# Optimization experiments

Hardware: AMD Instinct MI355X
Metric: run time of the kernel (lower is better)

The kernel has to match this reference:

```python
import jax, jax.numpy as jnp
import numpy as np

B, T, D, H, L, S = 128, 100, 256, 512, 40000, 10  # batch, steps, input_size, hidden_size, loc_count, num_slots


def setup_inputs() -> dict:
    key = jax.random.key(0)
    ks = jax.random.split(key, 24)
    stdv = 1.0 / np.sqrt(H)
    u = lambda k, shape: jax.random.uniform(k, shape, jnp.float32, -stdv, stdv)
    inp = {
        "batch_l": jax.random.randint(ks[0], (B, T), 0, L),
        "t_ld": jax.random.uniform(ks[1], (B, T), jnp.float32),
        "t_hd": jax.random.uniform(ks[2], (B, T), jnp.float32),
        "t_l": jax.random.randint(ks[3], (B, T), 0, S),
        "t_h": jax.random.randint(ks[4], (B, T), 0, S),
        "d_ld": jax.random.uniform(ks[5], (B, T), jnp.float32),
        "d_hd": jax.random.uniform(ks[6], (B, T), jnp.float32),
        "d_l": jax.random.randint(ks[7], (B, T), 0, S),
        "d_h": jax.random.randint(ks[8], (B, T), 0, S),
        # learned parameters
        "embed_l": jax.random.normal(ks[9], (L, D), jnp.float32) * 0.02,
        "embed_s": jax.random.normal(ks[10], (S, D), jnp.float32) * 0.02,
        "embed_q": jax.random.normal(ks[11], (S, D), jnp.float32) * 0.02,
        "w_ih": u(ks[12], (4 * H, D)),
        "w_hh": u(ks[13], (4 * H, H)),
        "w_s": u(ks[14], (3 * H, D)),
        "w_q": u(ks[15], (3 * H, D)),
        "b_ih": u(ks[16], (4 * H,)),
        "b_hh": u(ks[17], (4 * H,)),
        "w_out": u(ks[18], (L, H)),
        "b_out": u(ks[19], (L,)),
    }
    return inp


def reference(batch_l, t_ld, t_hd, t_l, t_h, d_ld, d_hd, d_l, d_h,
              embed_l, embed_s, embed_q, w_ih, w_hh, w_s, w_q,
              b_ih, b_hh, w_out, b_out):
    # embedding lookups + slot interpolation: lower_embed*hd + higher_embed*ld
    xl = embed_l[batch_l]                                           # (B,T,D)
    xs = embed_s[d_l] * d_hd[..., None] + embed_s[d_h] * d_ld[..., None]
    xq = embed_q[t_l] * t_hd[..., None] + embed_q[t_h] * t_ld[..., None]

    def step(hc, x):
        h, c = hc
        xl_t, xs_t, xq_t = x                                        # each (B,D)
        gates = xl_t @ w_ih.T + h @ w_hh.T + b_ih + b_hh            # (B,4H)
        i, f, g, o = jnp.split(gates, 4, axis=1)
        sq = xs_t @ w_s.T + xq_t @ w_q.T                            # (B,3H), order (i,f,o)
        si, sf, so = jnp.split(sq, 3, axis=1)
        i = jax.nn.sigmoid(i + si)
        f = jax.nn.sigmoid(f + sf)
        o = jax.nn.sigmoid(o + so)
        g = jnp.tanh(g)
        c2 = f * c + i * g
        h2 = o * jnp.tanh(g)  # faithful to source: tanh(cell_gate), not tanh(next_cell)
        return (h2, c2), None

    h0 = jnp.zeros((B, H), xl.dtype)
    (hT, cT), _ = jax.lax.scan(
        step, (h0, h0),
        (xl.transpose(1, 0, 2), xs.transpose(1, 0, 2), xq.transpose(1, 0, 2)))
    # classifier on last hidden state
    return hT @ w_out.T + b_out                                     # (B,L)
```

## Files before the change

kernel.cpp:

```cpp
#include <hip/hip_runtime.h>

#define B_ 128
#define T_ 100
#define D_ 256
#define H_ 512
#define L_ 40000
#define S_ 10

__device__ __forceinline__ float sigm_(float x){ return 1.f/(1.f + __expf(-x)); }
__device__ __forceinline__ float tanh_(float x){ return 1.f - 2.f/(__expf(2.f*x) + 1.f); }

typedef __attribute__((ext_vector_type(8))) short bf16x8;
typedef __attribute__((ext_vector_type(4))) float f32x4;

__device__ __forceinline__ unsigned short bfhi_(float x){
  unsigned u = __float_as_uint(x);
  return (unsigned short)((u + 0x7FFFu + ((u >> 16) & 1u)) >> 16);
}
__device__ __forceinline__ float bf2f_(unsigned short h){
  return __uint_as_float(((unsigned)h) << 16);
}
__device__ __forceinline__ float decp_(unsigned u){
  return bf2f_((unsigned short)(u & 0xFFFFu)) + bf2f_((unsigned short)(u >> 16));
}

__global__ void k_init(unsigned long long* __restrict__ h_enc, unsigned* __restrict__ flags,
                       const float* __restrict__ embed_s, const float* __restrict__ embed_q,
                       const float* __restrict__ w_s, const float* __restrict__ w_q,
                       float* __restrict__ es_proj, float* __restrict__ eq_proj){
  int bid = blockIdx.x, tid = threadIdx.x;
  if (bid < 256){ h_enc[bid*256 + tid] = 0ull; return; }
  if (bid == 256){ if (tid < 256) flags[tid] = 0u; return; }
  int b2 = bid - 257;
  int table = b2/20, rem = b2%20, s = rem/2, half = rem%2;
  int jo = half*256 + tid;
  const float* emb = (table ? embed_q : embed_s) + s*D_;
  const float* w   = (table ? w_q : w_s) + (size_t)(2*H_ + jo)*D_;
  float acc = 0.f;
  #pragma unroll 4
  for (int k=0;k<D_;++k) acc = fmaf(emb[k], w[k], acc);
  (table ? eq_proj : es_proj)[s*H_ + jo] = acc;
}

__global__ __launch_bounds__(256) void k_conv_w(
  const float* __restrict__ w_ih,
  unsigned short* __restrict__ Whi, unsigned short* __restrict__ Wlo)
{
  int g = blockIdx.x*256 + threadIdx.x;
  size_t row = (size_t)(g >> 6), k4 = (size_t)(g & 63)*4;
  const float* src = w_ih + (2*H_ + row)*D_ + k4;
  size_t off = row*D_ + k4;
  float4 v = *(const float4*)src;
  ushort4 hi, lo;
  hi.x = bfhi_(v.x); lo.x = bfhi_(v.x - bf2f_(hi.x));
  hi.y = bfhi_(v.y); lo.y = bfhi_(v.y - bf2f_(hi.y));
  hi.z = bfhi_(v.z); lo.z = bfhi_(v.z - bf2f_(hi.z));
  hi.w = bfhi_(v.w); lo.w = bfhi_(v.w - bf2f_(hi.w));
  *(ushort4*)(Whi + off) = hi;
  *(ushort4*)(Wlo + off) = lo;
}

__global__ __launch_bounds__(256,2) void k_phase1(
  const int* __restrict__ batch_l, const float* __restrict__ embed_l,
  const unsigned short* __restrict__ Whi, const unsigned short* __restrict__ Wlo,
  const float* __restrict__ b_ih, const float* __restrict__ b_hh,
  const float* __restrict__ t_ld, const float* __restrict__ t_hd,
  const int* __restrict__ t_l, const int* __restrict__ t_h,
  const float* __restrict__ d_ld, const float* __restrict__ d_hd,
  const int* __restrict__ d_l, const int* __restrict__ d_h,
  const float* __restrict__ es_proj, const float* __restrict__ eq_proj,
  float* __restrict__ P)
{
  __shared__ int ridx[64];
  int mt = blockIdx.x, jg = blockIdx.y;
  int t = mt >> 1, b0 = (mt & 1)*64;
  int tid = threadIdx.x;
  if (tid < 64) ridx[tid] = batch_l[(b0+tid)*T_ + t];
  __syncthreads();

  int lane = tid & 63, wv = tid >> 6;
  int ar = lane & 15, kb = lane >> 4;
  int mw = wv*16;
  f32x4 acc[16];
  #pragma unroll
  for (int nf=0;nf<16;++nf) acc[nf] = (f32x4){0.f,0.f,0.f,0.f};
  const float* arow_f = embed_l + (size_t)ridx[mw + ar]*D_ + kb*8;
  const size_t brow0 = (size_t)(jg*256 + ar)*D_ + kb*8;
  #pragma unroll
  for (int kc=0; kc<8; ++kc){
    float4 f0 = *(const float4*)(arow_f + kc*32);
    float4 f1 = *(const float4*)(arow_f + kc*32 + 4);
    float vv[8] = {f0.x,f0.y,f0.z,f0.w,f1.x,f1.y,f1.z,f1.w};
    bf16x8 a_hi, a_lo;
    #pragma unroll
    for (int i=0;i<8;++i){
      unsigned short h = bfhi_(vv[i]);
      a_hi[i] = (short)h;
      a_lo[i] = (short)bfhi_(vv[i] - bf2f_(h));
    }
    #pragma unroll
    for (int nf=0; nf<16; ++nf){
      bf16x8 b_hi = *(const bf16x8*)(Whi + brow0 + (size_t)nf*16*D_ + kc*32);
      bf16x8 b_lo = *(const bf16x8*)(Wlo + brow0 + (size_t)nf*16*D_ + kc*32);
      acc[nf] = __builtin_amdgcn_mfma_f32_16x16x32_bf16(a_hi, b_hi, acc[nf], 0, 0, 0);
      acc[nf] = __builtin_amdgcn_mfma_f32_16x16x32_bf16(a_hi, b_lo, acc[nf], 0, 0, 0);
      acc[nf] = __builtin_amdgcn_mfma_f32_16x16x32_bf16(a_lo, b_hi, acc[nf], 0, 0, 0);
    }
  }

  float bias[16];
  #pragma unroll
  for (int nf=0; nf<16; ++nf){
    int j = jg*256 + nf*16 + ar;
    bias[nf] = b_ih[2*H_ + j] + b_hh[2*H_ + j];
  }
  #pragma unroll
  for (int r=0; r<4; ++r){
    int b = b0 + mw + kb*4 + r;
    float dldv=0.f, dhdv=0.f, tldv=0.f, thdv=0.f;
    int dlv=0, dhv=0, tlv=0, thv=0;
    if (jg >= 2){
      int bt = b*T_ + t;
      dldv=d_ld[bt]; dhdv=d_hd[bt]; tldv=t_ld[bt]; thdv=t_hd[bt];
      dlv=d_l[bt]; dhv=d_h[bt]; tlv=t_l[bt]; thv=t_h[bt];
    }
    #pragma unroll
    for (int nf=0; nf<16; ++nf){
      int j = jg*256 + nf*16 + ar;
      float v = acc[nf][r] + bias[nf];
      if (jg >= 2){
        int jo = j - 512;
        v += dhdv*es_proj[dlv*H_+jo] + dldv*es_proj[dhv*H_+jo]
           + thdv*eq_proj[tlv*H_+jo] + tldv*eq_proj[thv*H_+jo];
      }
      P[((size_t)t*B_ + b)*1024 + j] = v;
    }
  }
}

__global__ __launch_bounds__(256,1) void k_rec(
  const float* __restrict__ w_hh, const float* __restrict__ P,
  unsigned long long* __restrict__ h_enc, unsigned* __restrict__ flags)
{
  extern __shared__ char smc[];
  unsigned short* Whi = (unsigned short*)smc;
  unsigned short* Wlo = Whi + 64*528;
  unsigned* hb = (unsigned*)(Wlo + 64*528);
  int bid = blockIdx.x;
  int bg = bid & 15, js = bid >> 4;
  int tid = threadIdx.x;
  int lane = tid & 63, wv = tid >> 6;
  const int gb0 = bg*8;
  unsigned* bgflags = flags + bg*16;

  {
    int r = tid >> 2;
    int c0 = (tid & 3)*128;
    int rr = r & 15;
    int jrow = js*32 + (r>>4)*8 + (rr & 7);
    const float* src = w_hh + (size_t)(((rr<8)?2:3)*H_ + jrow)*H_ + c0;
    unsigned short* dhi = Whi + r*528 + c0;
    unsigned short* dlo = Wlo + r*528 + c0;
    #pragma unroll 4
    for (int i=0;i<32;++i){
      float4 v = *(const float4*)(src + i*4);
      ushort4 hi, lo;
      hi.x=bfhi_(v.x); lo.x=bfhi_(v.x-bf2f_(hi.x));
      hi.y=bfhi_(v.y); lo.y=bfhi_(v.y-bf2f_(hi.y));
      hi.z=bfhi_(v.z); lo.z=bfhi_(v.z-bf2f_(hi.z));
      hi.w=bfhi_(v.w); lo.w=bfhi_(v.w-bf2f_(hi.w));
      *(ushort4*)(dhi + i*4) = hi;
      *(ushort4*)(dlo + i*4) = lo;
    }
  }

  const bool live = (lane < 32) && ((lane & 15) < 8);
  int bb = lane & 15;
  int j0l = js*32 + wv*8 + (lane>>4)*4;
  float pgv[4] = {0,0,0,0}, pov[4] = {0,0,0,0};
  if (live){
    size_t prow = (size_t)(gb0 + bb)*1024;
    float4 g4 = *(const float4*)&P[prow + j0l];
    float4 o4 = *(const float4*)&P[prow + 512 + j0l];
    pgv[0]=g4.x; pgv[1]=g4.y; pgv[2]=g4.z; pgv[3]=g4.w;
    pov[0]=o4.x; pov[1]=o4.y; pov[2]=o4.z; pov[3]=o4.w;
  }
  const int arow_off = (wv*16 + (lane & 15))*528 + (lane>>4)*8;
  const int hcol = lane & 7;
  const int hp0 = (lane>>4)*4;

  for (int t=0; t<T_; ++t){
    int par = t & 1;
    if (t > 0 && tid < 16){
      unsigned* f = bgflags + tid;
      int guard = 0;
      while (__hip_atomic_load(f, __ATOMIC_RELAXED, __HIP_MEMORY_SCOPE_AGENT) < (unsigned)t){
        __builtin_amdgcn_s_sleep(4);
        if (++guard > (1<<22)) break;
      }
    }
    __syncthreads();

    const unsigned long long* hsrc =
      h_enc + (size_t)par*(B_*H_/2) + (size_t)gb0*256 + tid;
    unsigned long long v[8];
    #pragma unroll
    for (int b=0;b<8;++b)
      v[b] = __hip_atomic_load(&hsrc[(size_t)b*256], __ATOMIC_RELAXED, __HIP_MEMORY_SCOPE_AGENT);
    {
      unsigned* r0 = hb + tid*18;
      *(uint2*)(r0+ 0) = make_uint2((unsigned)v[0],(unsigned)v[1]);
      *(uint2*)(r0+ 2) = make_uint2((unsigned)v[2],(unsigned)v[3]);
      *(uint2*)(r0+ 4) = make_uint2((unsigned)v[4],(unsigned)v[5]);
      *(uint2*)(r0+ 6) = make_uint2((unsigned)v[6],(unsigned)v[7]);
      *(uint2*)(r0+ 8) = make_uint2((unsigned)(v[0]>>32),(unsigned)(v[1]>>32));
      *(uint2*)(r0+10) = make_uint2((unsigned)(v[2]>>32),(unsigned)(v[3]>>32));
      *(uint2*)(r0+12) = make_uint2((unsigned)(v[4]>>32),(unsigned)(v[5]>>32));
      *(uint2*)(r0+14) = make_uint2((unsigned)(v[6]>>32),(unsigned)(v[7]>>32));
    }
    __syncthreads();

    f32x4 ac0 = {0,0,0,0}, ac1 = {0,0,0,0}, ac2 = {0,0,0,0};
    #pragma unroll
    for (int kc=0; kc<16; ++kc){
      bf16x8 bh, bl;
      #pragma unroll
      for (int e=0;e<8;++e){
        unsigned u = hb[(kc*16 + hp0 + (e>>1))*18 + (e&1)*8 + hcol];
        bh[e] = (short)(u & 0xFFFFu);
        bl[e] = (short)(u >> 16);
      }
      bf16x8 ah = *(const bf16x8*)(Whi + arow_off + kc*32);
      bf16x8 al = *(const bf16x8*)(Wlo + arow_off + kc*32);
      ac0 = __builtin_amdgcn_mfma_f32_16x16x32_bf16(ah, bh, ac0, 0, 0, 0);
      ac1 = __builtin_amdgcn_mfma_f32_16x16x32_bf16(ah, bl, ac1, 0, 0, 0);
      ac2 = __builtin_amdgcn_mfma_f32_16x16x32_bf16(al, bh, ac2, 0, 0, 0);
    }
    float accv[4], oov[4];
    #pragma unroll
    for (int r=0;r<4;++r) accv[r] = ac0[r] + ac1[r] + ac2[r];
    #pragma unroll
    for (int r=0;r<4;++r) oov[r] = __shfl_xor(accv[r], 32, 64);

    if (live){
      float h[4];
      #pragma unroll
      for (int r=0;r<4;++r){
        float gg = accv[r] + pgv[r];
        float oo = oov[r]  + pov[r];
        h[r] = sigm_(oo)*tanh_(tanh_(gg));
      }
      unsigned short p0h=bfhi_(h[0]), p0l=bfhi_(h[0]-bf2f_(p0h));
      unsigned short p1h=bfhi_(h[1]), p1l=bfhi_(h[1]-bf2f_(p1h));
      unsigned short p2h=bfhi_(h[2]), p2l=bfhi_(h[2]-bf2f_(p2h));
      unsigned short p3h=bfhi_(h[3]), p3l=bfhi_(h[3]-bf2f_(p3h));
      unsigned long long u0 = (unsigned long long)p0h | ((unsigned long long)p0l<<16)
                            | ((unsigned long long)p1h<<32) | ((unsigned long long)p1l<<48);
      unsigned long long u1 = (unsigned long long)p2h | ((unsigned long long)p2l<<16)
                            | ((unsigned long long)p3h<<32) | ((unsigned long long)p3l<<48);
      unsigned long long* dst =
        h_enc + (size_t)(1-par)*(B_*H_/2) + (size_t)(gb0 + bb)*256 + (j0l>>1);
      __hip_atomic_store(dst,   u0, __ATOMIC_RELAXED, __HIP_MEMORY_SCOPE_AGENT);
      __hip_atomic_store(dst+1, u1, __ATOMIC_RELAXED, __HIP_MEMORY_SCOPE_AGENT);
      if (t+1 < T_){
        size_t prow = ((size_t)(t+1)*B_ + gb0 + bb)*1024;
        float4 g4 = *(const float4*)&P[prow + j0l];
        float4 o4 = *(const float4*)&P[prow + 512 + j0l];
        pgv[0]=g4.x; pgv[1]=g4.y; pgv[2]=g4.z; pgv[3]=g4.w;
        pov[0]=o4.x; pov[1]=o4.y; pov[2]=o4.z; pov[3]=o4.w;
      }
    }
    __syncthreads();
    if (t+1 < T_ && tid == 0)
      __hip_atomic_store(bgflags + js, (unsigned)(t+1),
                         __ATOMIC_RELAXED, __HIP_MEMORY_SCOPE_AGENT);
  }
}

__global__ __launch_bounds__(256) void k_cls(
  const unsigned long long* __restrict__ h_enc, const float* __restrict__ w_out,
  const float* __restrict__ b_out, float* __restrict__ out)
{
  __shared__ float wt[32*68];
  __shared__ float htl[32*132];
  int l0 = blockIdx.x * 64;
  int tid = threadIdx.x;
  int lq = tid >> 4, bq = tid & 15;
  float acc[4][8] = {};
  for (int kc=0; kc<16; ++kc){
    int k0 = kc*32;
    __syncthreads();
    #pragma unroll
    for (int it=0; it<2; ++it){
      int f = it*256 + tid;
      int l = f >> 3, k4 = (f & 7)*4;
      float4 v = *(const float4*)&w_out[(size_t)(l0+l)*H_ + k0 + k4];
      wt[(k4+0)*68 + l] = v.x; wt[(k4+1)*68 + l] = v.y;
      wt[(k4+2)*68 + l] = v.z; wt[(k4+3)*68 + l] = v.w;
    }
    #pragma unroll
    for (int it=0; it<4; ++it){
      int f = it*256 + tid;
      int b = f >> 3, k4 = (f & 7)*4;
      uint4 v = *(const uint4*)&h_enc[(size_t)b*256 + ((k0 + k4) >> 1)];
      htl[(k4+0)*132 + b] = decp_(v.x);
      htl[(k4+1)*132 + b] = decp_(v.y);
      htl[(k4+2)*132 + b] = decp_(v.z);
      htl[(k4+3)*132 + b] = decp_(v.w);
    }
    __syncthreads();
    #pragma unroll 4
    for (int k=0;k<32;++k){
      float4 w4 = *(const float4*)&wt[k*68 + lq*4];
      float4 h0 = *(const float4*)&htl[k*132 + bq*8];
      float4 h1 = *(const float4*)&htl[k*132 + bq*8 + 4];
      float wv[4] = {w4.x,w4.y,w4.z,w4.w};
      float hv[8] = {h0.x,h0.y,h0.z,h0.w,h1.x,h1.y,h1.z,h1.w};
      #pragma unroll
      for (int m=0;m<4;++m)
        #pragma unroll
        for (int i=0;i<8;++i) acc[m][i] = fmaf(wv[m], hv[i], acc[m][i]);
    }
  }
  int l = l0 + lq*4;
  float4 bo = *(const float4*)&b_out[l];
  #pragma unroll
  for (int i=0;i<8;++i){
    int b = bq*8 + i;
    float4 o4;
    o4.x = acc[0][i] + bo.x; o4.y = acc[1][i] + bo.y;
    o4.z = acc[2][i] + bo.z; o4.w = acc[3][i] + bo.w;
    *(float4*)&out[(size_t)b*L_ + l] = o4;
  }
}

extern "C" void kernel_launch(void* const* d_in, const int* in_sizes, int n_in,
                              void* d_out, int out_size, void* d_ws, size_t ws_size,
                              hipStream_t stream) {
  const int*   batch_l = (const int*)  d_in[0];
  const float* t_ld    = (const float*)d_in[1];
  const float* t_hd    = (const float*)d_in[2];
  const int*   t_l     = (const int*)  d_in[3];
  const int*   t_h     = (const int*)  d_in[4];
  const float* d_ld    = (const float*)d_in[5];
  const float* d_hd    = (const float*)d_in[6];
  const int*   d_l     = (const int*)  d_in[7];
  const int*   d_h     = (const int*)  d_in[8];
  const float* embed_l = (const float*)d_in[9];
  const float* embed_s = (const float*)d_in[10];
  const float* embed_q = (const float*)d_in[11];
  const float* w_ih    = (const float*)d_in[12];
  const float* w_hh    = (const float*)d_in[13];
  const float* w_s     = (const float*)d_in[14];
  const float* w_q     = (const float*)d_in[15];
  const float* b_ih    = (const float*)d_in[16];
  const float* b_hh    = (const float*)d_in[17];
  const float* w_out   = (const float*)d_in[18];
  const float* b_out   = (const float*)d_in[19];
  float* out = (float*)d_out;

  float* ws = (float*)d_ws;
  const size_t P_off   = 0;
  const size_t h_off   = 13107200;
  const size_t es_off  = h_off + 131072;
  const size_t eq_off  = es_off + 5120;
  const size_t flg_off = eq_off + 5120;
  const size_t whi_off = flg_off + 256;
  const size_t wlo_off = whi_off + 131072;
  const size_t need_full = (wlo_off + 131072)*4 + 64;
  if (ws_size < need_full) return;

  float* P        = ws + P_off;
  unsigned long long* h_enc = (unsigned long long*)(ws + h_off);
  float* es_proj  = ws + es_off;
  float* eq_proj  = ws + eq_off;
  unsigned* flags = (unsigned*)(ws + flg_off);
  unsigned short* Whi = (unsigned short*)(ws + whi_off);
  unsigned short* Wlo = (unsigned short*)(ws + wlo_off);

  hipFuncSetAttribute(reinterpret_cast<const void*>(k_rec),
                      hipFuncAttributeMaxDynamicSharedMemorySize, 153600);

  k_init<<<297, 256, 0, stream>>>(h_enc, flags, embed_s, embed_q, w_s, w_q,
                                  es_proj, eq_proj);
  k_conv_w<<<256, 256, 0, stream>>>(w_ih, Whi, Wlo);
  k_phase1<<<dim3(200,4), 256, 0, stream>>>(batch_l, embed_l, Whi, Wlo,
      b_ih, b_hh, t_ld, t_hd, t_l, t_h, d_ld, d_hd, d_l, d_h, es_proj, eq_proj, P);
  k_rec<<<256, 256, 153600, stream>>>(w_hh, P, h_enc, flags);
  k_cls<<<625, 256, 0, stream>>>(h_enc, w_out, b_out, out);
}
```

Before: 564.3 us.

## Compute classifier GEMM with split-bf16 MFMA instead of scalar FMA

Rewrites the final classifier kernel to use bf16 MFMA 16x16x32 instructions. It emulates fp32 precision by splitting both the hidden state (already stored as hi/lo bf16 pairs) and w_out (converted on the fly) into high and low parts, then summing three products. w_out is now read straight from global memory into registers rather than staged through LDS, and the hidden tile is kept packed in LDS. The output stores become scattered scalar writes instead of float4. The change is meant to cut the FMA-bound cost of the 40000x128x512 GEMM, at the cost of per-element bf16 conversion work and less coalesced output writes.

```diff
diff --git a/kernel.cpp b/kernel.cpp
--- a/kernel.cpp
+++ b/kernel.cpp
@@ -19,9 +19,6 @@
 }
 __device__ __forceinline__ float bf2f_(unsigned short h){
   return __uint_as_float(((unsigned)h) << 16);
-}
-__device__ __forceinline__ float decp_(unsigned u){
-  return bf2f_((unsigned short)(u & 0xFFFFu)) + bf2f_((unsigned short)(u >> 16));
 }
 
 __global__ void k_init(unsigned long long* __restrict__ h_enc, unsigned* __restrict__ flags,
@@ -277,60 +274,82 @@
   }
 }
 
-__global__ __launch_bounds__(256) void k_cls(
+__global__ __launch_bounds__(256,2) void k_cls(
   const unsigned long long* __restrict__ h_enc, const float* __restrict__ w_out,
   const float* __restrict__ b_out, float* __restrict__ out)
 {
-  __shared__ float wt[32*68];
-  __shared__ float htl[32*132];
+  __shared__ unsigned hbA[128*132];
   int l0 = blockIdx.x * 64;
   int tid = threadIdx.x;
-  int lq = tid >> 4, bq = tid & 15;
-  float acc[4][8] = {};
-  for (int kc=0; kc<16; ++kc){
-    int k0 = kc*32;
+  int lane = tid & 63, wv = tid >> 6;
+  int cl = lane & 15;
+  int kb = lane >> 4;
+  f32x4 acc[2][4];
+  #pragma unroll
+  for (int m=0;m<2;++m)
+    #pragma unroll
+    for (int nf=0;nf<4;++nf) acc[m][nf] = (f32x4){0.f,0.f,0.f,0.f};
+
+  for (int kc=0; kc<4; ++kc){
     __syncthreads();
     #pragma unroll
-    for (int it=0; it<2; ++it){
-      int f = it*256 + tid;
-      int l = f >> 3, k4 = (f & 7)*4;
-      float4 v = *(const float4*)&w_out[(size_t)(l0+l)*H_ + k0 + k4];
-      wt[(k4+0)*68 + l] = v.x; wt[(k4+1)*68 + l] = v.y;
-      wt[(k4+2)*68 + l] = v.z; wt[(k4+3)*68 + l] = v.w;
-    }
-    #pragma unroll
-    for (int it=0; it<4; ++it){
-      int f = it*256 + tid;
-      int b = f >> 3, k4 = (f & 7)*4;
-      uint4 v = *(const uint4*)&h_enc[(size_t)b*256 + ((k0 + k4) >> 1)];
-      htl[(k4+0)*132 + b] = decp_(v.x);
-      htl[(k4+1)*132 + b] = decp_(v.y);
-      htl[(k4+2)*132 + b] = decp_(v.z);
-      htl[(k4+3)*132 + b] = decp_(v.w);
+    for (int it=0; it<32; ++it){
+      int g = it*256 + tid;
+      int b = g >> 6, i = g & 63;
+      unsigned long long v = h_enc[(size_t)b*256 + kc*64 + i];
+      *(uint2*)&hbA[b*132 + 2*i] = make_uint2((unsigned)v, (unsigned)(v>>32));
     }
     __syncthreads();
-    #pragma unroll 4
-    for (int k=0;k<32;++k){
-      float4 w4 = *(const float4*)&wt[k*68 + lq*4];
-      float4 h0 = *(const float4*)&htl[k*132 + bq*8];
-      float4 h1 = *(const float4*)&htl[k*132 + bq*8 + 4];
-      float wv[4] = {w4.x,w4.y,w4.z,w4.w};
-      float hv[8] = {h0.x,h0.y,h0.z,h0.w,h1.x,h1.y,h1.z,h1.w};
+    #pragma unroll
+    for (int ks=0; ks<4; ++ks){
+      bf16x8 ah[2], al[2];
       #pragma unroll
-      for (int m=0;m<4;++m)
+      for (int m=0;m<2;++m){
+        const unsigned* ap = &hbA[((2*wv+m)*16 + cl)*132 + ks*32 + kb*8];
         #pragma unroll
-        for (int i=0;i<8;++i) acc[m][i] = fmaf(wv[m], hv[i], acc[m][i]);
-    }
-  }
-  int l = l0 + lq*4;
-  float4 bo = *(const float4*)&b_out[l];
-  #pragma unroll
-  for (int i=0;i<8;++i){
-    int b = bq*8 + i;
-    float4 o4;
-    o4.x = acc[0][i] + bo.x; o4.y = acc[1][i] + bo.y;
-    o4.z = acc[2][i] + bo.z; o4.w = acc[3][i] + bo.w;
-    *(float4*)&out[(size_t)b*L_ + l] = o4;
+        for (int e=0;e<8;++e){
+          unsigned u = ap[e];
+          ah[m][e] = (short)(u & 0xFFFFu);
+          al[m][e] = (short)(u >> 16);
+        }
+      }
+      #pragma unroll
+      for (int nf=0; nf<4; ++nf){
+        const float* bp = w_out + (size_t)(l0 + nf*16 + cl)*H_ + kc*128 + ks*32 + kb*8;
+        float4 f0 = *(const float4*)bp;
+        float4 f1 = *(const float4*)(bp + 4);
+        float vvb[8] = {f0.x,f0.y,f0.z,f0.w,f1.x,f1.y,f1.z,f1.w};
+        bf16x8 bh, bl;
+        #pragma unroll
+        for (int e=0;e<8;++e){
+          unsigned short h = bfhi_(vvb[e]);
+          bh[e] = (short)h;
+          bl[e] = (short)bfhi_(vvb[e] - bf2f_(h));
+        }
+        #pragma unroll
+        for (int m=0;m<2;++m){
+          acc[m][nf] = __builtin_amdgcn_mfma_f32_16x16x32_bf16(ah[m], bh, acc[m][nf], 0, 0, 0);
+          acc[m][nf] = __builtin_amdgcn_mfma_f32_16x16x32_bf16(ah[m], bl, acc[m][nf], 0, 0, 0);
+          acc[m][nf] = __builtin_amdgcn_mfma_f32_16x16x32_bf16(al[m], bh, acc[m][nf], 0, 0, 0);
+        }
+      }
+    }
+  }
+
+  float bo[4];
+  #pragma unroll
+  for (int nf=0;nf<4;++nf) bo[nf] = b_out[l0 + nf*16 + cl];
+  #pragma unroll
+  for (int m=0;m<2;++m){
+    #pragma unroll
+    for (int r=0;r<4;++r){
+      int b = (2*wv + m)*16 + kb*4 + r;
+      #pragma unroll
+      for (int nf=0;nf<4;++nf){
+        int l = l0 + nf*16 + cl;
+        out[(size_t)b*L_ + l] = acc[m][nf][r] + bo[nf];
+      }
+    }
   }
 }
 
```

Result: slower. 609.0 us (+7.9%).

## Embed step tag in packed hidden state to replace flag-based barrier

Applied to the files above, without the earlier changes.

The hidden state is now stored as a 24-bit fixed-point value carrying an 8-bit timestep tag, plus a raw fp32 value, in each 64-bit word. Readers spin on the tag inside the data itself instead of relying only on the flag wait. The bf16 hi/lo split moves from the writer to the reader side. The flag wait still exists, so the added spin mainly guards ordering. The 24-bit fixed-point encoding loses precision and assumes |h|<1, and the 8-bit tag must not wrap within T=100 steps.

```diff
diff --git a/kernel.cpp b/kernel.cpp
--- a/kernel.cpp
+++ b/kernel.cpp
@@ -20,8 +20,9 @@
 __device__ __forceinline__ float bf2f_(unsigned short h){
   return __uint_as_float(((unsigned)h) << 16);
 }
-__device__ __forceinline__ float decp_(unsigned u){
-  return bf2f_((unsigned short)(u & 0xFFFFu)) + bf2f_((unsigned short)(u >> 16));
+__device__ __forceinline__ float dec24_(unsigned w){
+  int i = ((int)(w << 8)) >> 8;
+  return (float)i * 1.1920928955078125e-7f;
 }
 
 __global__ void k_init(unsigned long long* __restrict__ h_enc, unsigned* __restrict__ flags,
@@ -208,15 +209,43 @@
     for (int b=0;b<8;++b)
       v[b] = __hip_atomic_load(&hsrc[(size_t)b*256], __ATOMIC_RELAXED, __HIP_MEMORY_SCOPE_AGENT);
     {
+      unsigned want = (unsigned)t;
+      int guard = 0;
+      while (true){
+        int bad = 0;
+        #pragma unroll
+        for (int b=0;b<8;++b) bad |= ((((unsigned)v[b]) >> 24) != want) ? (1<<b) : 0;
+        if (!bad) break;
+        if (++guard > (1<<22)) break;
+        __builtin_amdgcn_s_sleep(1);
+        #pragma unroll
+        for (int b=0;b<8;++b)
+          if (bad & (1<<b))
+            v[b] = __hip_atomic_load(&hsrc[(size_t)b*256], __ATOMIC_RELAXED, __HIP_MEMORY_SCOPE_AGENT);
+      }
+    }
+    unsigned w0[8], w1[8];
+    #pragma unroll
+    for (int b=0;b<8;++b){
+      float f0 = dec24_((unsigned)v[b]);
+      float f1 = __uint_as_float((unsigned)(v[b] >> 32));
+      unsigned short h0h = bfhi_(f0);
+      unsigned short h0l = bfhi_(f0 - bf2f_(h0h));
+      unsigned short h1h = bfhi_(f1);
+      unsigned short h1l = bfhi_(f1 - bf2f_(h1h));
+      w0[b] = (unsigned)h0h | ((unsigned)h0l << 16);
+      w1[b] = (unsigned)h1h | ((unsigned)h1l << 16);
+    }
+    {
       unsigned* r0 = hb + tid*18;
-      *(uint2*)(r0+ 0) = make_uint2((unsigned)v[0],(unsigned)v[1]);
-      *(uint2*)(r0+ 2) = make_uint2((unsigned)v[2],(unsigned)v[3]);
-      *(uint2*)(r0+ 4) = make_uint2((unsigned)v[4],(unsigned)v[5]);
-      *(uint2*)(r0+ 6) = make_uint2((unsigned)v[6],(unsigned)v[7]);
-      *(uint2*)(r0+ 8) = make_uint2((unsigned)(v[0]>>32),(unsigned)(v[1]>>32));
-      *(uint2*)(r0+10) = make_uint2((unsigned)(v[2]>>32),(unsigned)(v[3]>>32));
-      *(uint2*)(r0+12) = make_uint2((unsigned)(v[4]>>32),(unsigned)(v[5]>>32));
-      *(uint2*)(r0+14) = make_uint2((unsigned)(v[6]>>32),(unsigned)(v[7]>>32));
+      *(uint2*)(r0+ 0) = make_uint2(w0[0],w0[1]);
+      *(uint2*)(r0+ 2) = make_uint2(w0[2],w0[3]);
+      *(uint2*)(r0+ 4) = make_uint2(w0[4],w0[5]);
+      *(uint2*)(r0+ 6) = make_uint2(w0[6],w0[7]);
+      *(uint2*)(r0+ 8) = make_uint2(w1[0],w1[1]);
+      *(uint2*)(r0+10) = make_uint2(w1[2],w1[3]);
+      *(uint2*)(r0+12) = make_uint2(w1[4],w1[5]);
+      *(uint2*)(r0+14) = make_uint2(w1[6],w1[7]);
     }
     __syncthreads();
 
@@ -250,14 +279,13 @@
         float oo = oov[r]  + pov[r];
         h[r] = sigm_(oo)*tanh_(tanh_(gg));
       }
-      unsigned short p0h=bfhi_(h[0]), p0l=bfhi_(h[0]-bf2f_(p0h));
-      unsigned short p1h=bfhi_(h[1]), p1l=bfhi_(h[1]-bf2f_(p1h));
-      unsigned short p2h=bfhi_(h[2]), p2l=bfhi_(h[2]-bf2f_(p2h));
-      unsigned short p3h=bfhi_(h[3]), p3l=bfhi_(h[3]-bf2f_(p3h));
-      unsigned long long u0 = (unsigned long long)p0h | ((unsigned long long)p0l<<16)
-                            | ((unsigned long long)p1h<<32) | ((unsigned long long)p1l<<48);
-      unsigned long long u1 = (unsigned long long)p2h | ((unsigned long long)p2l<<16)
-                            | ((unsigned long long)p3h<<32) | ((unsigned long long)p3l<<48);
+      unsigned tg = (unsigned)(t+1) << 24;
+      unsigned lo0 = ((unsigned)__float2int_rn(h[0] * 8388608.f) & 0xFFFFFFu) | tg;
+      unsigned long long u0 = (unsigned long long)lo0
+                            | ((unsigned long long)__float_as_uint(h[1]) << 32);
+      unsigned lo1 = ((unsigned)__float2int_rn(h[2] * 8388608.f) & 0xFFFFFFu) | tg;
+      unsigned long long u1 = (unsigned long long)lo1
+                            | ((unsigned long long)__float_as_uint(h[3]) << 32);
       unsigned long long* dst =
         h_enc + (size_t)(1-par)*(B_*H_/2) + (size_t)(gb0 + bb)*256 + (j0l>>1);
       __hip_atomic_store(dst,   u0, __ATOMIC_RELAXED, __HIP_MEMORY_SCOPE_AGENT);
@@ -303,10 +331,10 @@
       int f = it*256 + tid;
       int b = f >> 3, k4 = (f & 7)*4;
       uint4 v = *(const uint4*)&h_enc[(size_t)b*256 + ((k0 + k4) >> 1)];
-      htl[(k4+0)*132 + b] = decp_(v.x);
-      htl[(k4+1)*132 + b] = decp_(v.y);
-      htl[(k4+2)*132 + b] = decp_(v.z);
-      htl[(k4+3)*132 + b] = decp_(v.w);
+      htl[(k4+0)*132 + b] = dec24_(v.x);
+      htl[(k4+1)*132 + b] = __uint_as_float(v.y);
+      htl[(k4+2)*132 + b] = dec24_(v.z);
+      htl[(k4+3)*132 + b] = __uint_as_float(v.w);
     }
     __syncthreads();
     #pragma unroll 4
```

New measurement: 599.3 us. 1.06x slower.
